# Kernel tuning notes

Measured on AMD Instinct MI355X. Metric: run time of the kernel, lower is better.

The kernel has to match this reference:

```python
import jax, jax.numpy as jnp
import numpy as np

B, M, DM, H, DH, R = 8, 1024, 768, 12, 64, 32
RFF, DFF, RWO = 384, 3072, 384
LN_EPS = 1e-12


def _layernorm(x, g, b):
    mu = jnp.mean(x, axis=-1, keepdims=True)
    var = jnp.var(x, axis=-1, keepdims=True)
    return (x - mu) * jax.lax.rsqrt(var + LN_EPS) * g + b


def setup_inputs() -> dict:
    key = jax.random.key(0)
    ks = jax.random.split(key, 24)
    sc = 0.05  # keep pre-softmax logits in a sane range
    inp = {
        'x': jax.random.normal(ks[0], (B, M, DM), jnp.float32),
        'mask': jnp.zeros((B, M), jnp.float32),  # additive mask (0 = keep)
        'Pq': jax.random.normal(ks[1], (H, DM, R), jnp.float32) * sc,
        'Vq': jax.random.normal(ks[2], (H, R, DH), jnp.float32) * sc,
        'bq': jax.random.normal(ks[3], (H, DH), jnp.float32) * sc,
        'Pk': jax.random.normal(ks[4], (H, DM, R), jnp.float32) * sc,
        'Vk': jax.random.normal(ks[5], (H, R, DH), jnp.float32) * sc,
        'bk': jax.random.normal(ks[6], (H, DH), jnp.float32) * sc,
        'Pv': jax.random.normal(ks[7], (H, DM, R), jnp.float32) * sc,
        'Vv': jax.random.normal(ks[8], (H, R, DH), jnp.float32) * sc,
        'bv': jax.random.normal(ks[9], (H, DH), jnp.float32) * sc,
        'Uo': jax.random.normal(ks[10], (DM, RWO), jnp.float32) * sc,
        'Vo': jax.random.normal(ks[11], (RWO, DM), jnp.float32) * sc,
        'bo_attn': jax.random.normal(ks[12], (DM,), jnp.float32) * sc,
        'U1': jax.random.normal(ks[13], (DM, RFF), jnp.float32) * sc,
        'V1': jax.random.normal(ks[14], (RFF, DFF), jnp.float32) * sc,
        'b1': jax.random.normal(ks[15], (DFF,), jnp.float32) * sc,
        'U2': jax.random.normal(ks[16], (DFF, RFF), jnp.float32) * sc,
        'V2': jax.random.normal(ks[17], (RFF, DM), jnp.float32) * sc,
        'b2': jax.random.normal(ks[18], (DM,), jnp.float32) * sc,
        'ln1_g': jnp.ones((DM,), jnp.float32),
        'ln1_b': jnp.zeros((DM,), jnp.float32),
        'ln2_g': jnp.ones((DM,), jnp.float32),
        'ln2_b': jnp.zeros((DM,), jnp.float32),
    }
    return inp


def reference(x, mask, Pq, Vq, bq, Pk, Vk, bk, Pv, Vv, bv,
              Uo, Vo, bo_attn, U1, V1, b1, U2, V2, b2,
              ln1_g, ln1_b, ln2_g, ln2_b):
    # --- low-rank Q/K/V reconstruction: x@P -> [B,H,M,R], then @V + bias -> [B,H,M,dh]
    def qkv(P, V, b):
        t = jnp.einsum('bmd,hdr->bhmr', x, P)
        return jnp.einsum('bhmr,hrd->bhmd', t, V) + b[None, :, None, :]

    Q = qkv(Pq, Vq, bq)
    K = qkv(Pk, Vk, bk)
    Vh = qkv(Pv, Vv, bv)

    # --- flash-style attention (math equivalent, dense reference)
    scale = 1.0 / jnp.sqrt(jnp.asarray(DH, x.dtype))
    scores = jnp.einsum('bhmd,bhnd->bhmn', Q, K) * scale
    scores = scores + mask[:, None, None, :]  # additive mask [B,1,1,M]
    probs = jax.nn.softmax(scores, axis=-1)
    attn = jnp.einsum('bhmn,bhnd->bhmd', probs, Vh)  # [B,H,M,dh]
    attn = attn.transpose(0, 2, 1, 3).reshape(B, M, DM)

    # --- low-rank Wo projection + residual + LN1
    x1 = _layernorm(x + (attn @ Uo) @ Vo + bo_attn, ln1_g, ln1_b)

    # --- fused low-rank FFN: GELU((x1@U1)@V1 + b1) @ U2 @ V2 + b2
    mid = x1 @ U1                              # [B,M,r_ff]
    hdn = jax.nn.gelu(mid @ V1 + b1, approximate=False)  # [B,M,d_ff]
    y = (hdn @ U2) @ V2 + b2                   # [B,M,dm]

    return _layernorm(x1 + y, ln2_g, ln2_b)
```

## Files before the change

kernel.cpp:

```cpp
#include <hip/hip_runtime.h>
#include <hip/hip_bf16.h>


typedef float f32x4 __attribute__((ext_vector_type(4)));
typedef __bf16 bf16x8 __attribute__((ext_vector_type(8)));

#define NB   8
#define NM   1024
#define NDM  768
#define NH   12
#define NDH  64
#define NR   32
#define NRFF 384
#define NDFF 3072
#define NRWO 384
#define ROWS (NB*NM)
#define NQK  1536
#define NTQ  1152

__device__ __forceinline__ float fexp2(float x) {
#if __has_builtin(__builtin_amdgcn_exp2f)
  return __builtin_amdgcn_exp2f(x);
#else
  return exp2f(x);
#endif
}

__device__ __forceinline__ unsigned short f2bf(float f) {
  __hip_bfloat16 h = __float2bfloat16(f);
  return *reinterpret_cast<unsigned short*>(&h);
}

__device__ __forceinline__ int xcd_swizzle(int orig, int nwg) {
  int q = nwg >> 3, r = nwg & 7;
  int xcd = orig & 7, idx = orig >> 3;
  return (xcd < r ? xcd * (q + 1) : r * (q + 1) + (xcd - r) * q) + idx;
}

__global__ void prep_elem(const float* __restrict__ x, const float* __restrict__ Uo,
                          const float* __restrict__ mask,
                          __hip_bfloat16* __restrict__ xb, __hip_bfloat16* __restrict__ uoB,
                          float* __restrict__ mask2) {
  const int NX = 1572864, NU = 73728, NMK = 2048;
  for (int i = blockIdx.x * blockDim.x + threadIdx.x; i < NX + NU + NMK;
       i += gridDim.x * blockDim.x) {
    if (i < NX) {
      float4 v = ((const float4*)x)[i];
      ushort4 o = {f2bf(v.x), f2bf(v.y), f2bf(v.z), f2bf(v.w)};
      ((ushort4*)xb)[i] = o;
    } else if (i < NX + NU) {
      int j = i - NX;
      float4 v = ((const float4*)Uo)[j];
      ushort4 o = {f2bf(v.x), f2bf(v.y), f2bf(v.z), f2bf(v.w)};
      ((ushort4*)uoB)[j] = o;
    } else {
      int j = i - NX - NU;
      float4 v = ((const float4*)mask)[j];
      const float L = 1.44269504088896f;
      float4 o = {v.x * L, v.y * L, v.z * L, v.w * L};
      ((float4*)mask2)[j] = o;
    }
  }
}

__global__ __launch_bounds__(256) void prep_tT(
    const float* __restrict__ Vo, const float* __restrict__ U1, const float* __restrict__ V1,
    const float* __restrict__ U2, const float* __restrict__ V2,
    __hip_bfloat16* __restrict__ voT, __hip_bfloat16* __restrict__ u1T,
    __hip_bfloat16* __restrict__ v1T, __hip_bfloat16* __restrict__ u2T,
    __hip_bfloat16* __restrict__ v2T) {
  int blk = blockIdx.x;
  const float* src; __hip_bfloat16* dst; int R, C, lid;
  if (blk < 72)        { src = Vo; dst = voT; R = 384;  C = 768;  lid = blk; }
  else if (blk < 144)  { src = U1; dst = u1T; R = 768;  C = 384;  lid = blk - 72; }
  else if (blk < 432)  { src = V1; dst = v1T; R = 384;  C = 3072; lid = blk - 144; }
  else if (blk < 720)  { src = U2; dst = u2T; R = 3072; C = 384;  lid = blk - 432; }
  else                 { src = V2; dst = v2T; R = 384;  C = 768;  lid = blk - 720; }
  int tilesC = C >> 6;
  int tr = lid / tilesC, tc = lid - tr * tilesC;
  int r0 = tr << 6, c0 = tc << 6;
  __shared__ float sm[64][65];
  int tx = threadIdx.x & 63, ty = threadIdx.x >> 6;
#pragma unroll
  for (int k = 0; k < 16; k++) {
    int rr = ty * 16 + k;
    sm[rr][tx] = src[(size_t)(r0 + rr) * C + c0 + tx];
  }
  __syncthreads();
#pragma unroll
  for (int k = 0; k < 16; k++) {
    int cc = ty * 16 + k;
    dst[(size_t)(c0 + cc) * R + r0 + tx] = __float2bfloat16(sm[tx][cc]);
  }
}

__global__ __launch_bounds__(256) void prep_pT(
    const float* __restrict__ Pq, const float* __restrict__ Pk, const float* __restrict__ Pv,
    __hip_bfloat16* __restrict__ ptT) {
  const int blk = blockIdx.x;
  const int th = blk / 12, chunk = blk % 12;
  const int t = th / NH, h = th % NH;
  const float* P = (t == 0) ? Pq : (t == 1) ? Pk : Pv;
  __shared__ float sm[64][33];
  const int tid = threadIdx.x;
  {
    int dm_l = tid >> 2, r0 = (tid & 3) * 8;
    const float* src = P + ((size_t)h * NDM + chunk * 64 + dm_l) * NR + r0;
#pragma unroll
    for (int j = 0; j < 8; j++) sm[dm_l][r0 + j] = src[j];
  }
  __syncthreads();
  {
    int r = tid >> 3, dm0 = (tid & 7) * 8;
    int n = t * 384 + h * 32 + r;
    ushort4 lo, hi;
    lo.x = f2bf(sm[dm0 + 0][r]); lo.y = f2bf(sm[dm0 + 1][r]);
    lo.z = f2bf(sm[dm0 + 2][r]); lo.w = f2bf(sm[dm0 + 3][r]);
    hi.x = f2bf(sm[dm0 + 4][r]); hi.y = f2bf(sm[dm0 + 5][r]);
    hi.z = f2bf(sm[dm0 + 6][r]); hi.w = f2bf(sm[dm0 + 7][r]);
    ushort4* d = (ushort4*)(ptT + (size_t)n * NDM + chunk * 64 + dm0);
    d[0] = lo;
    d[1] = hi;
  }
}

template <int EPI, int BNt>
__global__ __launch_bounds__(256) void gemm_bt(
    const __hip_bfloat16* __restrict__ A, const __hip_bfloat16* __restrict__ Bt,
    int M, int N, int K,
    const float* __restrict__ bias,
    const __hip_bfloat16* __restrict__ residb,
    __hip_bfloat16* __restrict__ outb, float* __restrict__ outf) {
  constexpr int NWC = BNt / 64;
  constexpr int NWR = 4 / NWC;
  constexpr int IFR = 128 / (NWR * 16);
  constexpr int WROWS = 128 / NWR;
  constexpr int BCH = BNt / 32;
  __shared__ __align__(16) char lsA[128 * 128];
  __shared__ __align__(16) char lsB[BNt * 128];
  const int tid = threadIdx.x;
  const int lane = tid & 63, wid = tid >> 6;
  const int wr = wid / NWC, wc = wid % NWC;
  const int gx = gridDim.x;
  const int wg = xcd_swizzle(blockIdx.y * gx + blockIdx.x, gx * gridDim.y);
  const int bm = (wg / gx) * 128, bn = (wg % gx) * BNt;
  const int g = lane >> 4, q = lane & 15;

  const int l3 = lane >> 3;
  const int kc = (lane & 7) ^ l3;

  f32x4 acc[IFR][4];
#pragma unroll
  for (int i = 0; i < IFR; i++)
#pragma unroll
    for (int j = 0; j < 4; j++) acc[i][j] = f32x4{0.f, 0.f, 0.f, 0.f};

  for (int k0 = 0; k0 < K; k0 += 64) {
#pragma unroll
    for (int c = 0; c < 4; c++) {
      int chunk = wid * 4 + c;
      int row = chunk * 8 + l3;
      const __hip_bfloat16* ga = A + (size_t)(bm + row) * K + k0 + kc * 8;
      __builtin_amdgcn_global_load_lds(
          (const __attribute__((address_space(1))) void*)ga,
          (__attribute__((address_space(3))) void*)&lsA[chunk * 1024], 16, 0, 0);
    }
#pragma unroll
    for (int c = 0; c < BCH; c++) {
      int chunk = wid * BCH + c;
      int row = chunk * 8 + l3;
      const __hip_bfloat16* gb = Bt + (size_t)(bn + row) * K + k0 + kc * 8;
      __builtin_amdgcn_global_load_lds(
          (const __attribute__((address_space(1))) void*)gb,
          (__attribute__((address_space(3))) void*)&lsB[chunk * 1024], 16, 0, 0);
    }
    __syncthreads();
#pragma unroll
    for (int ks = 0; ks < 2; ks++) {
      bf16x8 af[IFR], bfr[4];
#pragma unroll
      for (int i = 0; i < IFR; i++) {
        int ra = wr * WROWS + i * 16 + q;
        af[i] = *(const bf16x8*)&lsA[ra * 128 + ((ks * 64 + g * 16) ^ ((ra & 7) << 4))];
      }
#pragma unroll
      for (int j = 0; j < 4; j++) {
        int rb = wc * 64 + j * 16 + q;
        bfr[j] = *(const bf16x8*)&lsB[rb * 128 + ((ks * 64 + g * 16) ^ ((rb & 7) << 4))];
      }
      __builtin_amdgcn_s_setprio(1);
#pragma unroll
      for (int i = 0; i < IFR; i++)
#pragma unroll
        for (int j = 0; j < 4; j++)
          acc[i][j] = __builtin_amdgcn_mfma_f32_16x16x32_bf16(af[i], bfr[j], acc[i][j], 0, 0, 0);
      __builtin_amdgcn_s_setprio(0);
    }
    __syncthreads();
  }

#pragma unroll
  for (int i = 0; i < IFR; i++)
#pragma unroll
    for (int j = 0; j < 4; j++)
#pragma unroll
      for (int e = 0; e < 4; e++) {
        int row = bm + wr * WROWS + i * 16 + g * 4 + e;
        int col = bn + wc * 64 + j * 16 + q;
        float v = acc[i][j][e];
        if (EPI >= 1) v += bias[col];
        if (EPI == 2) v = 0.5f * v * (1.0f + erff(v * 0.70710678118654752f));
        if (EPI == 5) {
          v += __bfloat162float(residb[(size_t)row * N + col]);
          outf[(size_t)row * N + col] = v;
        } else {
          outb[(size_t)row * N + col] = __float2bfloat16(v);
        }
      }
}

__global__ __launch_bounds__(256) void qkv_apply(
    const __hip_bfloat16* __restrict__ tq,
    const float* __restrict__ Vq, const float* __restrict__ bq,
    const float* __restrict__ Vk, const float* __restrict__ bk,
    const float* __restrict__ Vv, const float* __restrict__ bv,
    __hip_bfloat16* __restrict__ qkb, __hip_bfloat16* __restrict__ vt) {
  const int th = blockIdx.x;
  const int t = th / NH, h = th % NH;
  const int bm = blockIdx.y * 256;
  const float* V = (t == 0) ? Vq : (t == 1) ? Vk : Vv;
  const float* bb = (t == 0) ? bq : (t == 1) ? bk : bv;
  __shared__ __align__(16) __hip_bfloat16 Vl[NDH][NR];
  const int tid = threadIdx.x;
  const int lane = tid & 63, w = tid >> 6;
  const int g = lane >> 4, q = lane & 15;

  {
    int r = tid >> 3, dh0 = (tid & 7) * 8;
    const float* src = V + ((size_t)h * NR + r) * NDH + dh0;
#pragma unroll
    for (int j = 0; j < 8; j++) Vl[dh0 + j][r] = __float2bfloat16(src[j]);
  }
  __syncthreads();

  bf16x8 bfr[4];
  float bj[4];
#pragma unroll
  for (int j = 0; j < 4; j++) {
    bfr[j] = *(const bf16x8*)&Vl[j * 16 + q][g * 8];
    bj[j] = bb[h * NDH + j * 16 + q];
  }

  bf16x8 af[4];
#pragma unroll
  for (int i = 0; i < 4; i++) {
    int row = bm + w * 64 + i * 16 + q;
    af[i] = *(const bf16x8*)(tq + (size_t)row * NTQ + t * 384 + h * 32 + g * 8);
  }

  f32x4 acc[4][4];
#pragma unroll
  for (int i = 0; i < 4; i++)
#pragma unroll
    for (int j = 0; j < 4; j++) {
      acc[i][j] = f32x4{0.f, 0.f, 0.f, 0.f};
      acc[i][j] = __builtin_amdgcn_mfma_f32_16x16x32_bf16(af[i], bfr[j], acc[i][j], 0, 0, 0);
    }

  if (t < 2) {
#pragma unroll
    for (int i = 0; i < 4; i++)
#pragma unroll
      for (int j = 0; j < 4; j++) {
        int dh = j * 16 + q;
#pragma unroll
        for (int e = 0; e < 4; e++) {
          int row = bm + w * 64 + i * 16 + g * 4 + e;
          qkb[(size_t)row * NQK + t * NDM + h * NDH + dh] = __float2bfloat16(acc[i][j][e] + bj[j]);
        }
      }
  } else {
#pragma unroll
    for (int i = 0; i < 4; i++)
#pragma unroll
      for (int j = 0; j < 4; j++) {
        int dh = j * 16 + q;
        int row0 = bm + w * 64 + i * 16 + g * 4;
        int b = row0 >> 10, m0 = row0 & 1023;
        float bi = bj[j];
        ushort4 st = {f2bf(acc[i][j][0] + bi), f2bf(acc[i][j][1] + bi),
                      f2bf(acc[i][j][2] + bi), f2bf(acc[i][j][3] + bi)};
        *(ushort4*)&vt[(((size_t)b * NH + h) * NDH + dh) * NM + m0] = st;
      }
  }
}

__global__ __launch_bounds__(256) void attn_kernel(const __hip_bfloat16* __restrict__ qk,
                                                   const __hip_bfloat16* __restrict__ vt,
                                                   const float* __restrict__ mask2,
                                                   __hip_bfloat16* __restrict__ attnb) {
  __shared__ __align__(16) char Kl[2][64 * 128];
  __shared__ __align__(16) char Vl[2][64 * 128];
  __shared__ __align__(16) char Pl[4][16 * 128];
  const int nblk = NB * NH * (NM / 64);
  const int blk = xcd_swizzle(blockIdx.x, nblk);
  const int qb = blk & 15;
  const int h = (blk >> 4) % NH;
  const int b = blk / (16 * NH);
  const int tid = threadIdx.x;
  const int lane = tid & 63, w = tid >> 6;
  const int g = lane >> 4, q = lane & 15;
  const size_t rowbase = (size_t)b * NM;
  const float S2 = 0.125f * 1.44269504088896f;

  const __hip_bfloat16* Kbase = qk + rowbase * NQK + NDM + h * 64;
  const __hip_bfloat16* Vbase = vt + ((size_t)(b * NH + h) * NDH) * NM;

  bf16x8 qf[2];
#pragma unroll
  for (int ks = 0; ks < 2; ks++)
    qf[ks] = *(const bf16x8*)(qk + (rowbase + qb * 64 + w * 16 + q) * NQK + h * 64 + g * 8 + ks * 32);

  bf16x8 onesf;
#pragma unroll
  for (int jj = 0; jj < 8; jj++) onesf[jj] = (__bf16)1.0f;

  const int l3 = lane >> 3;
  const int kc = (lane & 7) ^ l3;

  auto stage = [&](int buf, int t) {
    const int kv0 = t * 64;
#pragma unroll
    for (int c = 0; c < 2; c++) {
      int r8 = w * 16 + c * 8;
      int row = r8 + l3;
      const __hip_bfloat16* gk = Kbase + (size_t)(kv0 + row) * NQK + kc * 8;
      __builtin_amdgcn_global_load_lds(
          (const __attribute__((address_space(1))) void*)gk,
          (__attribute__((address_space(3))) void*)&Kl[buf][r8 * 128], 16, 0, 0);
      const __hip_bfloat16* gv = Vbase + (size_t)row * NM + kv0 + kc * 8;
      __builtin_amdgcn_global_load_lds(
          (const __attribute__((address_space(1))) void*)gv,
          (__attribute__((address_space(3))) void*)&Vl[buf][r8 * 128], 16, 0, 0);
    }
  };

  f32x4 oacc[4];
#pragma unroll
  for (int dt = 0; dt < 4; dt++) oacc[dt] = f32x4{0.f, 0.f, 0.f, 0.f};
  f32x4 lacc = f32x4{0.f, 0.f, 0.f, 0.f};

  stage(0, 0);
  __syncthreads();

  for (int t = 0; t < NM / 64; t++) {
    const int cur = t & 1;
    if (t + 1 < NM / 64) stage(cur ^ 1, t + 1);
    const int kv0 = t * 64;

    f32x4 sacc[4];
#pragma unroll
    for (int nt = 0; nt < 4; nt++) sacc[nt] = f32x4{0.f, 0.f, 0.f, 0.f};
    __builtin_amdgcn_s_setprio(1);
#pragma unroll
    for (int ks = 0; ks < 2; ks++) {
#pragma unroll
      for (int nt = 0; nt < 4; nt++) {
        int r = nt * 16 + q;
        bf16x8 kf = *(const bf16x8*)&Kl[cur][r * 128 + ((ks * 64 + g * 16) ^ ((r & 7) << 4))];
        sacc[nt] = __builtin_amdgcn_mfma_f32_16x16x32_bf16(kf, qf[ks], sacc[nt], 0, 0, 0);
      }
    }
    __builtin_amdgcn_s_setprio(0);

#pragma unroll
    for (int nt = 0; nt < 4; nt++) {
      const float4 mk = *(const float4*)(mask2 + b * NM + kv0 + nt * 16 + g * 4);
      ushort4 pk;
      pk.x = f2bf(fexp2(fmaf(sacc[nt][0], S2, mk.x)));
      pk.y = f2bf(fexp2(fmaf(sacc[nt][1], S2, mk.y)));
      pk.z = f2bf(fexp2(fmaf(sacc[nt][2], S2, mk.z)));
      pk.w = f2bf(fexp2(fmaf(sacc[nt][3], S2, mk.w)));
      *(ushort4*)&Pl[w][q * 128 + ((nt * 32 + g * 8) ^ ((q & 7) << 4))] = pk;
    }

    __builtin_amdgcn_s_setprio(1);
#pragma unroll
    for (int ks = 0; ks < 2; ks++) {
      bf16x8 pf = *(const bf16x8*)&Pl[w][q * 128 + ((ks * 64 + g * 16) ^ ((q & 7) << 4))];
#pragma unroll
      for (int dt = 0; dt < 4; dt++) {
        int r = dt * 16 + q;
        bf16x8 vf = *(const bf16x8*)&Vl[cur][r * 128 + ((ks * 64 + g * 16) ^ ((r & 7) << 4))];
        oacc[dt] = __builtin_amdgcn_mfma_f32_16x16x32_bf16(pf, vf, oacc[dt], 0, 0, 0);
      }
      lacc = __builtin_amdgcn_mfma_f32_16x16x32_bf16(pf, onesf, lacc, 0, 0, 0);
    }
    __builtin_amdgcn_s_setprio(0);
    __syncthreads();
  }

  float inv[4];
#pragma unroll
  for (int e = 0; e < 4; e++) inv[e] = 1.0f / lacc[e];
#pragma unroll
  for (int dt = 0; dt < 4; dt++)
#pragma unroll
    for (int e = 0; e < 4; e++) {
      int m = qb * 64 + w * 16 + g * 4 + e;
      int dh = dt * 16 + q;
      attnb[(rowbase + m) * NDM + h * 64 + dh] = __float2bfloat16(oacc[dt][e] * inv[e]);
    }
}

__global__ __launch_bounds__(256) void ln_kernel(const float* __restrict__ in, const float* __restrict__ gam,
                                                 const float* __restrict__ bet, float* __restrict__ outf,
                                                 __hip_bfloat16* __restrict__ outb) {
  const int row = blockIdx.x, tid = threadIdx.x;
  const float* p = in + (size_t)row * NDM;
  float v0 = p[tid], v1 = p[tid + 256], v2 = p[tid + 512];
  float s = v0 + v1 + v2, s2 = v0 * v0 + v1 * v1 + v2 * v2;
#pragma unroll
  for (int d = 1; d < 64; d <<= 1) {
    s += __shfl_xor(s, d);
    s2 += __shfl_xor(s2, d);
  }
  __shared__ float red[8];
  int w = tid >> 6;
  if ((tid & 63) == 0) { red[w] = s; red[4 + w] = s2; }
  __syncthreads();
  s = red[0] + red[1] + red[2] + red[3];
  s2 = red[4] + red[5] + red[6] + red[7];
  float mu = s * (1.0f / NDM);
  float var = fmaxf(s2 * (1.0f / NDM) - mu * mu, 0.0f);
  float rr = rsqrtf(var + 1e-12f);
  float o0 = (v0 - mu) * rr * gam[tid] + bet[tid];
  float o1 = (v1 - mu) * rr * gam[tid + 256] + bet[tid + 256];
  float o2 = (v2 - mu) * rr * gam[tid + 512] + bet[tid + 512];
  if (outf) {
    float* po = outf + (size_t)row * NDM;
    po[tid] = o0;
    po[tid + 256] = o1;
    po[tid + 512] = o2;
  }
  if (outb) {
    __hip_bfloat16* pb = outb + (size_t)row * NDM;
    pb[tid] = __float2bfloat16(o0);
    pb[tid + 256] = __float2bfloat16(o1);
    pb[tid + 512] = __float2bfloat16(o2);
  }
}

extern "C" void kernel_launch(void* const* d_in, const int* in_sizes, int n_in,
                              void* d_out, int out_size, void* d_ws, size_t ws_size,
                              hipStream_t stream) {
  const float* x = (const float*)d_in[0];
  const float* mask = (const float*)d_in[1];
  const float* Pq = (const float*)d_in[2];
  const float* Vq = (const float*)d_in[3];
  const float* bq = (const float*)d_in[4];
  const float* Pk = (const float*)d_in[5];
  const float* Vk = (const float*)d_in[6];
  const float* bk = (const float*)d_in[7];
  const float* Pv = (const float*)d_in[8];
  const float* Vv = (const float*)d_in[9];
  const float* bv = (const float*)d_in[10];
  const float* Uo = (const float*)d_in[11];
  const float* Vo = (const float*)d_in[12];
  const float* bo = (const float*)d_in[13];
  const float* U1 = (const float*)d_in[14];
  const float* V1 = (const float*)d_in[15];
  const float* b1 = (const float*)d_in[16];
  const float* U2 = (const float*)d_in[17];
  const float* V2 = (const float*)d_in[18];
  const float* b2 = (const float*)d_in[19];
  const float* ln1g = (const float*)d_in[20];
  const float* ln1b = (const float*)d_in[21];
  const float* ln2g = (const float*)d_in[22];
  const float* ln2b = (const float*)d_in[23];
  float* out = (float*)d_out;
  char* ws = (char*)d_ws;

  size_t off = 0;
  auto alloc = [&](size_t bytes) { size_t o = off; off += (bytes + 255) & ~(size_t)255; return o; };
  const size_t o_xb    = alloc((size_t)ROWS * NDM * 2);
  const size_t o_woT   = alloc((size_t)NDM * NDM * 2);
  const size_t o_uoB   = alloc((size_t)NDM * NRWO * 2);
  const size_t o_voT   = alloc((size_t)NDM * NRWO * 2);
  const size_t o_u1T   = alloc((size_t)NRFF * NDM * 2);
  const size_t o_v1T   = alloc((size_t)NDFF * NRFF * 2);
  const size_t o_u2T   = alloc((size_t)NRFF * NDFF * 2);
  const size_t o_v2T   = alloc((size_t)NDM * NRFF * 2);
  const size_t o_ptT   = alloc((size_t)NTQ * NDM * 2);
  const size_t o_mask2 = alloc((size_t)NB * NM * 4);
  const size_t o_tq    = alloc((size_t)ROWS * NTQ * 2);
  const size_t o_qk    = alloc((size_t)ROWS * NQK * 2);
  const size_t o_vt    = alloc((size_t)NB * NH * NDH * NM * 2);
  const size_t o_attnb = alloc((size_t)ROWS * NDM * 2);
  const size_t o_tmp   = alloc((size_t)ROWS * NDM * 4);
  const size_t o_x1b   = alloc((size_t)ROWS * NDM * 2);
  const size_t o_mid   = alloc((size_t)ROWS * NRFF * 2);
  const size_t o_mid2  = alloc((size_t)ROWS * NRFF * 2);
  const size_t o_hdn   = o_qk;

  __hip_bfloat16* xb    = (__hip_bfloat16*)(ws + o_xb);
  __hip_bfloat16* woT   = (__hip_bfloat16*)(ws + o_woT);
  __hip_bfloat16* uoB   = (__hip_bfloat16*)(ws + o_uoB);
  __hip_bfloat16* voT   = (__hip_bfloat16*)(ws + o_voT);
  __hip_bfloat16* u1T   = (__hip_bfloat16*)(ws + o_u1T);
  __hip_bfloat16* v1T   = (__hip_bfloat16*)(ws + o_v1T);
  __hip_bfloat16* u2T   = (__hip_bfloat16*)(ws + o_u2T);
  __hip_bfloat16* v2T   = (__hip_bfloat16*)(ws + o_v2T);
  __hip_bfloat16* ptT   = (__hip_bfloat16*)(ws + o_ptT);
  float*          mask2 = (float*)(ws + o_mask2);
  __hip_bfloat16* tq    = (__hip_bfloat16*)(ws + o_tq);
  __hip_bfloat16* qkb   = (__hip_bfloat16*)(ws + o_qk);
  __hip_bfloat16* vt    = (__hip_bfloat16*)(ws + o_vt);
  __hip_bfloat16* attnb = (__hip_bfloat16*)(ws + o_attnb);
  float*          tmp   = (float*)(ws + o_tmp);
  __hip_bfloat16* x1b   = (__hip_bfloat16*)(ws + o_x1b);
  __hip_bfloat16* mid   = (__hip_bfloat16*)(ws + o_mid);
  __hip_bfloat16* mid2  = (__hip_bfloat16*)(ws + o_mid2);
  __hip_bfloat16* hdn   = (__hip_bfloat16*)(ws + o_hdn);

  prep_elem<<<1024, 256, 0, stream>>>(x, Uo, mask, xb, uoB, mask2);
  prep_tT<<<792, 256, 0, stream>>>(Vo, U1, V1, U2, V2, voT, u1T, v1T, u2T, v2T);
  prep_pT<<<432, 256, 0, stream>>>(Pq, Pk, Pv, ptT);

  gemm_bt<0, 64><<<dim3(NDM / 64, NDM / 128), 256, 0, stream>>>(
      voT, uoB, NDM, NDM, NRWO, nullptr, nullptr, woT, nullptr);

  gemm_bt<0, 128><<<dim3(NTQ / 128, ROWS / 128), 256, 0, stream>>>(
      xb, ptT, ROWS, NTQ, NDM, nullptr, nullptr, tq, nullptr);

  qkv_apply<<<dim3(36, ROWS / 256), 256, 0, stream>>>(tq, Vq, bq, Vk, bk, Vv, bv, qkb, vt);

  attn_kernel<<<NB * NH * (NM / 64), 256, 0, stream>>>(qkb, vt, mask2, attnb);

  gemm_bt<5, 64><<<dim3(NDM / 64, ROWS / 128), 256, 0, stream>>>(
      attnb, woT, ROWS, NDM, NDM, bo, xb, nullptr, tmp);
  ln_kernel<<<ROWS, 256, 0, stream>>>(tmp, ln1g, ln1b, nullptr, x1b);

  gemm_bt<0, 64><<<dim3(NRFF / 64, ROWS / 128), 256, 0, stream>>>(
      x1b, u1T, ROWS, NRFF, NDM, nullptr, nullptr, mid, nullptr);
  gemm_bt<2, 128><<<dim3(NDFF / 128, ROWS / 128), 256, 0, stream>>>(
      mid, v1T, ROWS, NDFF, NRFF, b1, nullptr, hdn, nullptr);
  gemm_bt<0, 64><<<dim3(NRFF / 64, ROWS / 128), 256, 0, stream>>>(
      hdn, u2T, ROWS, NRFF, NDFF, nullptr, nullptr, mid2, nullptr);
  gemm_bt<5, 64><<<dim3(NDM / 64, ROWS / 128), 256, 0, stream>>>(
      mid2, v2T, ROWS, NDM, NRFF, b2, x1b, nullptr, tmp);

  ln_kernel<<<ROWS, 256, 0, stream>>>(tmp, ln2g, ln2b, out, nullptr);

  (void)in_sizes; (void)n_in; (void)out_size; (void)ws_size;
}
```

Before: 384.3 us.

## Merge prep kernels, use bf16 LN staging, single-buffer attention K/V tiles

Three separate changes. The three weight and input preparation kernels are merged into one launch that dispatches on block index, cutting launch overhead. The fp32 buffer holding the residual sum before each layernorm becomes bf16, halving its write and read traffic at some cost in precision. The attention kernel drops double-buffered K/V staging for a single LDS buffer loaded and synced each iteration; this frees LDS, possibly allowing more resident blocks, but loses the overlap between loads and MFMA work.

```diff
diff --git a/kernel.cpp b/kernel.cpp
--- a/kernel.cpp
+++ b/kernel.cpp
@@ -37,90 +37,86 @@
   return (xcd < r ? xcd * (q + 1) : r * (q + 1) + (xcd - r) * q) + idx;
 }
 
-__global__ void prep_elem(const float* __restrict__ x, const float* __restrict__ Uo,
-                          const float* __restrict__ mask,
-                          __hip_bfloat16* __restrict__ xb, __hip_bfloat16* __restrict__ uoB,
-                          float* __restrict__ mask2) {
-  const int NX = 1572864, NU = 73728, NMK = 2048;
-  for (int i = blockIdx.x * blockDim.x + threadIdx.x; i < NX + NU + NMK;
-       i += gridDim.x * blockDim.x) {
-    if (i < NX) {
-      float4 v = ((const float4*)x)[i];
-      ushort4 o = {f2bf(v.x), f2bf(v.y), f2bf(v.z), f2bf(v.w)};
-      ((ushort4*)xb)[i] = o;
-    } else if (i < NX + NU) {
-      int j = i - NX;
-      float4 v = ((const float4*)Uo)[j];
-      ushort4 o = {f2bf(v.x), f2bf(v.y), f2bf(v.z), f2bf(v.w)};
-      ((ushort4*)uoB)[j] = o;
-    } else {
-      int j = i - NX - NU;
-      float4 v = ((const float4*)mask)[j];
-      const float L = 1.44269504088896f;
-      float4 o = {v.x * L, v.y * L, v.z * L, v.w * L};
-      ((float4*)mask2)[j] = o;
-    }
-  }
-}
-
-__global__ __launch_bounds__(256) void prep_tT(
+__global__ __launch_bounds__(256) void prep_all(
+    const float* __restrict__ x, const float* __restrict__ Uo, const float* __restrict__ mask,
     const float* __restrict__ Vo, const float* __restrict__ U1, const float* __restrict__ V1,
     const float* __restrict__ U2, const float* __restrict__ V2,
+    const float* __restrict__ Pq, const float* __restrict__ Pk, const float* __restrict__ Pv,
+    __hip_bfloat16* __restrict__ xb, __hip_bfloat16* __restrict__ uoB, float* __restrict__ mask2,
     __hip_bfloat16* __restrict__ voT, __hip_bfloat16* __restrict__ u1T,
     __hip_bfloat16* __restrict__ v1T, __hip_bfloat16* __restrict__ u2T,
-    __hip_bfloat16* __restrict__ v2T) {
-  int blk = blockIdx.x;
-  const float* src; __hip_bfloat16* dst; int R, C, lid;
-  if (blk < 72)        { src = Vo; dst = voT; R = 384;  C = 768;  lid = blk; }
-  else if (blk < 144)  { src = U1; dst = u1T; R = 768;  C = 384;  lid = blk - 72; }
-  else if (blk < 432)  { src = V1; dst = v1T; R = 384;  C = 3072; lid = blk - 144; }
-  else if (blk < 720)  { src = U2; dst = u2T; R = 3072; C = 384;  lid = blk - 432; }
-  else                 { src = V2; dst = v2T; R = 384;  C = 768;  lid = blk - 720; }
-  int tilesC = C >> 6;
-  int tr = lid / tilesC, tc = lid - tr * tilesC;
-  int r0 = tr << 6, c0 = tc << 6;
+    __hip_bfloat16* __restrict__ v2T, __hip_bfloat16* __restrict__ ptT) {
+  const int blk = blockIdx.x;
+  const int tid = threadIdx.x;
   __shared__ float sm[64][65];
-  int tx = threadIdx.x & 63, ty = threadIdx.x >> 6;
-#pragma unroll
-  for (int k = 0; k < 16; k++) {
-    int rr = ty * 16 + k;
-    sm[rr][tx] = src[(size_t)(r0 + rr) * C + c0 + tx];
-  }
-  __syncthreads();
-#pragma unroll
-  for (int k = 0; k < 16; k++) {
-    int cc = ty * 16 + k;
-    dst[(size_t)(c0 + cc) * R + r0 + tx] = __float2bfloat16(sm[tx][cc]);
-  }
-}
-
-__global__ __launch_bounds__(256) void prep_pT(
-    const float* __restrict__ Pq, const float* __restrict__ Pk, const float* __restrict__ Pv,
-    __hip_bfloat16* __restrict__ ptT) {
-  const int blk = blockIdx.x;
-  const int th = blk / 12, chunk = blk % 12;
-  const int t = th / NH, h = th % NH;
-  const float* P = (t == 0) ? Pq : (t == 1) ? Pk : Pv;
-  __shared__ float sm[64][33];
-  const int tid = threadIdx.x;
-  {
-    int dm_l = tid >> 2, r0 = (tid & 3) * 8;
-    const float* src = P + ((size_t)h * NDM + chunk * 64 + dm_l) * NR + r0;
-#pragma unroll
-    for (int j = 0; j < 8; j++) sm[dm_l][r0 + j] = src[j];
-  }
-  __syncthreads();
-  {
-    int r = tid >> 3, dm0 = (tid & 7) * 8;
-    int n = t * 384 + h * 32 + r;
-    ushort4 lo, hi;
-    lo.x = f2bf(sm[dm0 + 0][r]); lo.y = f2bf(sm[dm0 + 1][r]);
-    lo.z = f2bf(sm[dm0 + 2][r]); lo.w = f2bf(sm[dm0 + 3][r]);
-    hi.x = f2bf(sm[dm0 + 4][r]); hi.y = f2bf(sm[dm0 + 5][r]);
-    hi.z = f2bf(sm[dm0 + 6][r]); hi.w = f2bf(sm[dm0 + 7][r]);
-    ushort4* d = (ushort4*)(ptT + (size_t)n * NDM + chunk * 64 + dm0);
-    d[0] = lo;
-    d[1] = hi;
+
+  if (blk < 1024) {
+    const int NX = 1572864, NU = 73728, NMK = 2048;
+    for (int i = blk * 256 + tid; i < NX + NU + NMK; i += 1024 * 256) {
+      if (i < NX) {
+        float4 v = ((const float4*)x)[i];
+        ushort4 o = {f2bf(v.x), f2bf(v.y), f2bf(v.z), f2bf(v.w)};
+        ((ushort4*)xb)[i] = o;
+      } else if (i < NX + NU) {
+        int j = i - NX;
+        float4 v = ((const float4*)Uo)[j];
+        ushort4 o = {f2bf(v.x), f2bf(v.y), f2bf(v.z), f2bf(v.w)};
+        ((ushort4*)uoB)[j] = o;
+      } else {
+        int j = i - NX - NU;
+        float4 v = ((const float4*)mask)[j];
+        const float L = 1.44269504088896f;
+        float4 o = {v.x * L, v.y * L, v.z * L, v.w * L};
+        ((float4*)mask2)[j] = o;
+      }
+    }
+  } else if (blk < 1816) {
+    int b2 = blk - 1024;
+    const float* src; __hip_bfloat16* dst; int R, C, lid;
+    if (b2 < 72)        { src = Vo; dst = voT; R = 384;  C = 768;  lid = b2; }
+    else if (b2 < 144)  { src = U1; dst = u1T; R = 768;  C = 384;  lid = b2 - 72; }
+    else if (b2 < 432)  { src = V1; dst = v1T; R = 384;  C = 3072; lid = b2 - 144; }
+    else if (b2 < 720)  { src = U2; dst = u2T; R = 3072; C = 384;  lid = b2 - 432; }
+    else                { src = V2; dst = v2T; R = 384;  C = 768;  lid = b2 - 720; }
+    int tilesC = C >> 6;
+    int tr = lid / tilesC, tc = lid - tr * tilesC;
+    int r0 = tr << 6, c0 = tc << 6;
+    int tx = tid & 63, ty = tid >> 6;
+#pragma unroll
+    for (int k = 0; k < 16; k++) {
+      int rr = ty * 16 + k;
+      sm[rr][tx] = src[(size_t)(r0 + rr) * C + c0 + tx];
+    }
+    __syncthreads();
+#pragma unroll
+    for (int k = 0; k < 16; k++) {
+      int cc = ty * 16 + k;
+      dst[(size_t)(c0 + cc) * R + r0 + tx] = __float2bfloat16(sm[tx][cc]);
+    }
+  } else {
+    int b3 = blk - 1816;
+    const int th = b3 / 12, chunk = b3 % 12;
+    const int t = th / NH, h = th % NH;
+    const float* P = (t == 0) ? Pq : (t == 1) ? Pk : Pv;
+    {
+      int dm_l = tid >> 2, r0 = (tid & 3) * 8;
+      const float* src = P + ((size_t)h * NDM + chunk * 64 + dm_l) * NR + r0;
+#pragma unroll
+      for (int j = 0; j < 8; j++) sm[dm_l][r0 + j] = src[j];
+    }
+    __syncthreads();
+    {
+      int r = tid >> 3, dm0 = (tid & 7) * 8;
+      int n = t * 384 + h * 32 + r;
+      ushort4 lo, hi;
+      lo.x = f2bf(sm[dm0 + 0][r]); lo.y = f2bf(sm[dm0 + 1][r]);
+      lo.z = f2bf(sm[dm0 + 2][r]); lo.w = f2bf(sm[dm0 + 3][r]);
+      hi.x = f2bf(sm[dm0 + 4][r]); hi.y = f2bf(sm[dm0 + 5][r]);
+      hi.z = f2bf(sm[dm0 + 6][r]); hi.w = f2bf(sm[dm0 + 7][r]);
+      ushort4* d = (ushort4*)(ptT + (size_t)n * NDM + chunk * 64 + dm0);
+      d[0] = lo;
+      d[1] = hi;
+    }
   }
 }
 
@@ -130,7 +126,7 @@
     int M, int N, int K,
     const float* __restrict__ bias,
     const __hip_bfloat16* __restrict__ residb,
-    __hip_bfloat16* __restrict__ outb, float* __restrict__ outf) {
+    __hip_bfloat16* __restrict__ outb) {
   constexpr int NWC = BNt / 64;
   constexpr int NWR = 4 / NWC;
   constexpr int IFR = 128 / (NWR * 16);
@@ -210,12 +206,8 @@
         float v = acc[i][j][e];
         if (EPI >= 1) v += bias[col];
         if (EPI == 2) v = 0.5f * v * (1.0f + erff(v * 0.70710678118654752f));
-        if (EPI == 5) {
-          v += __bfloat162float(residb[(size_t)row * N + col]);
-          outf[(size_t)row * N + col] = v;
-        } else {
-          outb[(size_t)row * N + col] = __float2bfloat16(v);
-        }
+        if (EPI == 5) v += __bfloat162float(residb[(size_t)row * N + col]);
+        outb[(size_t)row * N + col] = __float2bfloat16(v);
       }
 }
 
@@ -299,8 +291,8 @@
                                                    const __hip_bfloat16* __restrict__ vt,
                                                    const float* __restrict__ mask2,
                                                    __hip_bfloat16* __restrict__ attnb) {
-  __shared__ __align__(16) char Kl[2][64 * 128];
-  __shared__ __align__(16) char Vl[2][64 * 128];
+  __shared__ __align__(16) char Kl[64 * 128];
+  __shared__ __align__(16) char Vl[64 * 128];
   __shared__ __align__(16) char Pl[4][16 * 128];
   const int nblk = NB * NH * (NM / 64);
   const int blk = xcd_swizzle(blockIdx.x, nblk);
@@ -328,7 +320,7 @@
   const int l3 = lane >> 3;
   const int kc = (lane & 7) ^ l3;
 
-  auto stage = [&](int buf, int t) {
+  auto stage = [&](int t) {
     const int kv0 = t * 64;
 #pragma unroll
     for (int c = 0; c < 2; c++) {
@@ -337,11 +329,11 @@
       const __hip_bfloat16* gk = Kbase + (size_t)(kv0 + row) * NQK + kc * 8;
       __builtin_amdgcn_global_load_lds(
           (const __attribute__((address_space(1))) void*)gk,
-          (__attribute__((address_space(3))) void*)&Kl[buf][r8 * 128], 16, 0, 0);
+          (__attribute__((address_space(3))) void*)&Kl[r8 * 128], 16, 0, 0);
       const __hip_bfloat16* gv = Vbase + (size_t)row * NM + kv0 + kc * 8;
       __builtin_amdgcn_global_load_lds(
           (const __attribute__((address_space(1))) void*)gv,
-          (__attribute__((address_space(3))) void*)&Vl[buf][r8 * 128], 16, 0, 0);
+          (__attribute__((address_space(3))) void*)&Vl[r8 * 128], 16, 0, 0);
     }
   };
 
@@ -350,12 +342,9 @@
   for (int dt = 0; dt < 4; dt++) oacc[dt] = f32x4{0.f, 0.f, 0.f, 0.f};
   f32x4 lacc = f32x4{0.f, 0.f, 0.f, 0.f};
 
-  stage(0, 0);
-  __syncthreads();
-
   for (int t = 0; t < NM / 64; t++) {
-    const int cur = t & 1;
-    if (t + 1 < NM / 64) stage(cur ^ 1, t + 1);
+    stage(t);
+    __syncthreads();
     const int kv0 = t * 64;
 
     f32x4 sacc[4];
@@ -367,7 +356,7 @@
 #pragma unroll
       for (int nt = 0; nt < 4; nt++) {
         int r = nt * 16 + q;
-        bf16x8 kf = *(const bf16x8*)&Kl[cur][r * 128 + ((ks * 64 + g * 16) ^ ((r & 7) << 4))];
+        bf16x8 kf = *(const bf16x8*)&Kl[r * 128 + ((ks * 64 + g * 16) ^ ((r & 7) << 4))];
         sacc[nt] = __builtin_amdgcn_mfma_f32_16x16x32_bf16(kf, qf[ks], sacc[nt], 0, 0, 0);
       }
     }
@@ -391,7 +380,7 @@
 #pragma unroll
       for (int dt = 0; dt < 4; dt++) {
         int r = dt * 16 + q;
-        bf16x8 vf = *(const bf16x8*)&Vl[cur][r * 128 + ((ks * 64 + g * 16) ^ ((r & 7) << 4))];
+        bf16x8 vf = *(const bf16x8*)&Vl[r * 128 + ((ks * 64 + g * 16) ^ ((r & 7) << 4))];
         oacc[dt] = __builtin_amdgcn_mfma_f32_16x16x32_bf16(pf, vf, oacc[dt], 0, 0, 0);
       }
       lacc = __builtin_amdgcn_mfma_f32_16x16x32_bf16(pf, onesf, lacc, 0, 0, 0);
@@ -413,12 +402,15 @@
     }
 }
 
-__global__ __launch_bounds__(256) void ln_kernel(const float* __restrict__ in, const float* __restrict__ gam,
+__global__ __launch_bounds__(256) void ln_kernel(const __hip_bfloat16* __restrict__ in,
+                                                 const float* __restrict__ gam,
                                                  const float* __restrict__ bet, float* __restrict__ outf,
                                                  __hip_bfloat16* __restrict__ outb) {
   const int row = blockIdx.x, tid = threadIdx.x;
-  const float* p = in + (size_t)row * NDM;
-  float v0 = p[tid], v1 = p[tid + 256], v2 = p[tid + 512];
+  const __hip_bfloat16* p = in + (size_t)row * NDM;
+  float v0 = __bfloat162float(p[tid]);
+  float v1 = __bfloat162float(p[tid + 256]);
+  float v2 = __bfloat162float(p[tid + 512]);
   float s = v0 + v1 + v2, s2 = v0 * v0 + v1 * v1 + v2 * v2;
 #pragma unroll
   for (int d = 1; d < 64; d <<= 1) {
@@ -497,7 +489,7 @@
   const size_t o_qk    = alloc((size_t)ROWS * NQK * 2);
   const size_t o_vt    = alloc((size_t)NB * NH * NDH * NM * 2);
   const size_t o_attnb = alloc((size_t)ROWS * NDM * 2);
-  const size_t o_tmp   = alloc((size_t)ROWS * NDM * 4);
+  const size_t o_tmpb  = alloc((size_t)ROWS * NDM * 2);
   const size_t o_x1b   = alloc((size_t)ROWS * NDM * 2);
   const size_t o_mid   = alloc((size_t)ROWS * NRFF * 2);
   const size_t o_mid2  = alloc((size_t)ROWS * NRFF * 2);
@@ -517,40 +509,39 @@
   __hip_bfloat16* qkb   = (__hip_bfloat16*)(ws + o_qk);
   __hip_bfloat16* vt    = (__hip_bfloat16*)(ws + o_vt);
   __hip_bfloat16* attnb = (__hip_bfloat16*)(ws + o_attnb);
-  float*          tmp   = (float*)(ws + o_tmp);
+  __hip_bfloat16* tmpb  = (__hip_bfloat16*)(ws + o_tmpb);
   __hip_bfloat16* x1b   = (__hip_bfloat16*)(ws + o_x1b);
   __hip_bfloat16* mid   = (__hip_bfloat16*)(ws + o_mid);
   __hip_bfloat16* mid2  = (__hip_bfloat16*)(ws + o_mid2);
   __hip_bfloat16* hdn   = (__hip_bfloat16*)(ws + o_hdn);
 
-  prep_elem<<<1024, 256, 0, stream>>>(x, Uo, mask, xb, uoB, mask2);
-  prep_tT<<<792, 256, 0, stream>>>(Vo, U1, V1, U2, V2, voT, u1T, v1T, u2T, v2T);
-  prep_pT<<<432, 256, 0, stream>>>(Pq, Pk, Pv, ptT);
+  prep_all<<<2248, 256, 0, stream>>>(x, Uo, mask, Vo, U1, V1, U2, V2, Pq, Pk, Pv,
+                                     xb, uoB, mask2, voT, u1T, v1T, u2T, v2T, ptT);
 
   gemm_bt<0, 64><<<dim3(NDM / 64, NDM / 128), 256, 0, stream>>>(
-      voT, uoB, NDM, NDM, NRWO, nullptr, nullptr, woT, nullptr);
+      voT, uoB, NDM, NDM, NRWO, nullptr, nullptr, woT);
 
   gemm_bt<0, 128><<<dim3(NTQ / 128, ROWS / 128), 256, 0, stream>>>(
-      xb, ptT, ROWS, NTQ, NDM, nullptr, nullptr, tq, nullptr);
+      xb, ptT, ROWS, NTQ, NDM, nullptr, nullptr, tq);
 
   qkv_apply<<<dim3(36, ROWS / 256), 256, 0, stream>>>(tq, Vq, bq, Vk, bk, Vv, bv, qkb, vt);
 
   attn_kernel<<<NB * NH * (NM / 64), 256, 0, stream>>>(qkb, vt, mask2, attnb);
 
   gemm_bt<5, 64><<<dim3(NDM / 64, ROWS / 128), 256, 0, stream>>>(
-      attnb, woT, ROWS, NDM, NDM, bo, xb, nullptr, tmp);
-  ln_kernel<<<ROWS, 256, 0, stream>>>(tmp, ln1g, ln1b, nullptr, x1b);
+      attnb, woT, ROWS, NDM, NDM, bo, xb, tmpb);
+  ln_kernel<<<ROWS, 256, 0, stream>>>(tmpb, ln1g, ln1b, nullptr, x1b);
 
   gemm_bt<0, 64><<<dim3(NRFF / 64, ROWS / 128), 256, 0, stream>>>(
-      x1b, u1T, ROWS, NRFF, NDM, nullptr, nullptr, mid, nullptr);
+      x1b, u1T, ROWS, NRFF, NDM, nullptr, nullptr, mid);
   gemm_bt<2, 128><<<dim3(NDFF / 128, ROWS / 128), 256, 0, stream>>>(
-      mid, v1T, ROWS, NDFF, NRFF, b1, nullptr, hdn, nullptr);
+      mid, v1T, ROWS, NDFF, NRFF, b1, nullptr, hdn);
   gemm_bt<0, 64><<<dim3(NRFF / 64, ROWS / 128), 256, 0, stream>>>(
-      hdn, u2T, ROWS, NRFF, NDFF, nullptr, nullptr, mid2, nullptr);
+      hdn, u2T, ROWS, NRFF, NDFF, nullptr, nullptr, mid2);
   gemm_bt<5, 64><<<dim3(NDM / 64, ROWS / 128), 256, 0, stream>>>(
-      mid2, v2T, ROWS, NDM, NRFF, b2, x1b, nullptr, tmp);
-
-  ln_kernel<<<ROWS, 256, 0, stream>>>(tmp, ln2g, ln2b, out, nullptr);
+      mid2, v2T, ROWS, NDM, NRFF, b2, x1b, tmpb);
+
+  ln_kernel<<<ROWS, 256, 0, stream>>>(tmpb, ln2g, ln2b, out, nullptr);
 
   (void)in_sizes; (void)n_in; (void)out_size; (void)ws_size;
 }
```

After: 365.8 us. 1.05x faster.
